# Optimization experiments

Hardware: AMD Instinct MI355X
Metric: run time of the kernel (lower is better)

The kernel has to match this reference:

```python
import jax, jax.numpy as jnp
import numpy as np

N_NODES = 100000
N_EDGES = 1600000
D_FEAT = 64
EPS = 1e-07


def setup_inputs() -> dict:
    key = jax.random.key(0)
    k1, k2, k3 = jax.random.split(key, 3)
    x = jax.random.normal(k1, (N_NODES, D_FEAT), dtype=jnp.float32)
    beta = jnp.ones((1,), dtype=jnp.float32)
    edge_row = jnp.sort(jax.random.randint(k2, (N_EDGES,), 0, N_NODES, dtype=jnp.int64))
    edge_col = jax.random.randint(k3, (N_EDGES,), 0, N_NODES, dtype=jnp.int64)
    return {"x": x, "beta": beta, "edge_row": edge_row, "edge_col": edge_col}


def reference(x, beta, edge_row, edge_col):
    # Gather endpoint features: [E, d]
    A = x[edge_row]
    B = x[edge_col]
    # Cosine similarity per edge, scaled by beta: [E]
    inner = jnp.sum(A * B, axis=1)
    norms = jnp.linalg.norm(A, axis=1) * jnp.linalg.norm(B, axis=1)
    sim = beta[0] * (inner / (norms + EPS))
    # Sparse row-wise softmax (tf.sparse.softmax): stable segment softmax over edges grouped by row
    row_max = jax.ops.segment_max(sim, edge_row, num_segments=N_NODES)
    e = jnp.exp(sim - row_max[edge_row])
    row_sum = jax.ops.segment_sum(e, edge_row, num_segments=N_NODES)
    p = e / row_sum[edge_row]  # [E]
    # SPMM: out[i] = sum_{(i,j) in E} p_ij * x[j]
    out = jax.ops.segment_sum(p[:, None] * B, edge_row, num_segments=N_NODES)
    return out
```

## Files before the change

### kernel.cpp

```cpp
#include <hip/hip_runtime.h>
#include <math.h>

#define D_FEAT 64
typedef _Float16 v8h __attribute__((ext_vector_type(8)));
typedef float v4f __attribute__((ext_vector_type(4)));
typedef _Float16 h2 __attribute__((ext_vector_type(2)));

__device__ __forceinline__ v8h u2h8(uint4 u) { v8h v; __builtin_memcpy(&v, &u, 16); return v; }

__global__ __launch_bounds__(256)
void agnn_prep(const float* __restrict__ x, float* __restrict__ rn,
               uint2* __restrict__ xh, const int* __restrict__ edge_row,
               int* __restrict__ row_ptr, int n_nodes, int n_edges, int nb_prep) {
    if ((int)blockIdx.x < nb_prep) {
        int t = blockIdx.x * blockDim.x + threadIdx.x;
        int node = t >> 4;
        if (node >= n_nodes) return;
        int l4 = t & 15;
        float4 v = ((const float4*)x)[node * 16 + l4];
        float ss = v.x*v.x + v.y*v.y + v.z*v.z + v.w*v.w;
        #pragma unroll
        for (int off = 1; off < 16; off <<= 1) ss += __shfl_xor(ss, off, 64);
        if (l4 == 0) rn[node] = ss > 0.f ? rsqrtf(ss) : 0.f;
        h2 h0 = {(_Float16)v.x, (_Float16)v.y};
        h2 h1 = {(_Float16)v.z, (_Float16)v.w};
        uint2 u;
        __builtin_memcpy(&u.x, &h0, 4);
        __builtin_memcpy(&u.y, &h1, 4);
        xh[node * 16 + l4] = u;
    } else {
        int e = (blockIdx.x - nb_prep) * blockDim.x + threadIdx.x;
        if (e >= n_edges) return;
        int r1 = edge_row[e];
        int r0 = (e == 0) ? -1 : edge_row[e - 1];
        for (int r = r0 + 1; r <= r1; ++r) row_ptr[r] = e;
        if (e == n_edges - 1)
            for (int r = r1 + 1; r <= n_nodes; ++r) row_ptr[r] = n_edges;
    }
}

#define XCP_PITCH 144
#define P_PITCH    80
#define WAVE_LDS  (32 * XCP_PITCH + 16 * P_PITCH)

__global__ __launch_bounds__(64)
void agnn_fused(const float* __restrict__ beta_p,
                const int* __restrict__ edge_col,
                const int* __restrict__ row_ptr,
                const float* __restrict__ rn,
                const uint4* __restrict__ xh4,
                float* __restrict__ out, int n_nodes) {
    __shared__ char lds_raw[WAVE_LDS];
    int lane = threadIdx.x & 63;
    int q    = lane >> 4;
    int lo4  = lane & 15;
    char* XCP = lds_raw;
    char* PL  = XCP + 32 * XCP_PITCH;

    int tile = blockIdx.x;
    int t0 = tile * 16;
    if (t0 >= n_nodes) return;

    int qnode = t0 + lo4; if (qnode >= n_nodes) qnode = n_nodes - 1;
    v8h a0 = u2h8(xh4[(size_t)qnode * 8 + q]);
    v8h a1 = u2h8(xh4[(size_t)qnode * 8 + 4 + q]);

    float beta  = beta_p[0];
    float shift = fabsf(beta);
    int rb = t0 + q * 4;
    float brn0, brn1, brn2, brn3;
    if (t0 + 16 <= n_nodes) {
        float4 rq = *(const float4*)(rn + rb);
        brn0 = beta * rq.x; brn1 = beta * rq.y; brn2 = beta * rq.z; brn3 = beta * rq.w;
    } else {
        brn0 = beta * rn[min(rb + 0, n_nodes - 1)];
        brn1 = beta * rn[min(rb + 1, n_nodes - 1)];
        brn2 = beta * rn[min(rb + 2, n_nodes - 1)];
        brn3 = beta * rn[min(rb + 3, n_nodes - 1)];
    }

    int es   = row_ptr[t0];
    int tend = t0 + 16; if (tend > n_nodes) tend = n_nodes;
    int L    = row_ptr[tend] - es;

    int b0 = row_ptr[min(rb + 0, n_nodes)] - es;
    int b1 = row_ptr[min(rb + 1, n_nodes)] - es;
    int b2 = row_ptr[min(rb + 2, n_nodes)] - es;
    int b3 = row_ptr[min(rb + 3, n_nodes)] - es;
    int b4 = row_ptr[min(rb + 4, n_nodes)] - es;

    v4f o0 = {0,0,0,0}, o1 = {0,0,0,0}, o2 = {0,0,0,0}, o3 = {0,0,0,0};
    float l0 = 0.f, l1 = 0.f, l2 = 0.f, l3 = 0.f;
    unsigned int selp = (lo4 & 1) ? 0x07060302u : 0x05040100u;

    int nch = (L + 31) >> 5;
    if (nch > 0) {
        int cc0, cc1;
        {
            int i0 = lo4, i1 = lo4 + 16;
            cc0 = edge_col[es + (i0 < L ? i0 : 0)];
            cc1 = edge_col[es + (i1 < L ? i1 : 0)];
        }
        float rc0 = rn[cc0], rc1 = rn[cc1];
        uint4 A00 = xh4[(size_t)cc0 * 8 + q];
        uint4 A01 = xh4[(size_t)cc0 * 8 + 4 + q];
        uint4 A10 = xh4[(size_t)cc1 * 8 + q];
        uint4 A11 = xh4[(size_t)cc1 * 8 + 4 + q];

        for (int ch = 0; ch < nch; ++ch) {
            int base = ch << 5;
            bool more = (ch + 1) < nch;

            int nc0, nc1;
            if (more) {
                int i0 = base + 32 + lo4, i1 = i0 + 16;
                nc0 = edge_col[es + (i0 < L ? i0 : 0)];
                nc1 = edge_col[es + (i1 < L ? i1 : 0)];
            } else { nc0 = cc0; nc1 = cc1; }

            v4f z0 = {0,0,0,0};
            z0 = __builtin_amdgcn_mfma_f32_16x16x32_f16(a0, u2h8(A00), z0, 0, 0, 0);
            z0 = __builtin_amdgcn_mfma_f32_16x16x32_f16(a1, u2h8(A01), z0, 0, 0, 0);
            v4f z1 = {0,0,0,0};
            z1 = __builtin_amdgcn_mfma_f32_16x16x32_f16(a0, u2h8(A10), z1, 0, 0, 0);
            z1 = __builtin_amdgcn_mfma_f32_16x16x32_f16(a1, u2h8(A11), z1, 0, 0, 0);

            {
                unsigned int colA = lo4 * 4, colB = (16 + lo4) * 4;
                char* pA = XCP + (4 * q) * XCP_PITCH;
                char* pB = XCP + (16 + 4 * q) * XCP_PITCH;
                *(unsigned int*)(pA + 0 * XCP_PITCH + colA) = A00.x;
                *(unsigned int*)(pA + 1 * XCP_PITCH + colA) = A00.y;
                *(unsigned int*)(pA + 2 * XCP_PITCH + colA) = A00.z;
                *(unsigned int*)(pA + 3 * XCP_PITCH + colA) = A00.w;
                *(unsigned int*)(pB + 0 * XCP_PITCH + colA) = A01.x;
                *(unsigned int*)(pB + 1 * XCP_PITCH + colA) = A01.y;
                *(unsigned int*)(pB + 2 * XCP_PITCH + colA) = A01.z;
                *(unsigned int*)(pB + 3 * XCP_PITCH + colA) = A01.w;
                *(unsigned int*)(pA + 0 * XCP_PITCH + colB) = A10.x;
                *(unsigned int*)(pA + 1 * XCP_PITCH + colB) = A10.y;
                *(unsigned int*)(pA + 2 * XCP_PITCH + colB) = A10.z;
                *(unsigned int*)(pA + 3 * XCP_PITCH + colB) = A10.w;
                *(unsigned int*)(pB + 0 * XCP_PITCH + colB) = A11.x;
                *(unsigned int*)(pB + 1 * XCP_PITCH + colB) = A11.y;
                *(unsigned int*)(pB + 2 * XCP_PITCH + colB) = A11.z;
                *(unsigned int*)(pB + 3 * XCP_PITCH + colB) = A11.w;
            }

            float nr0, nr1; uint4 B00, B01, B10, B11;
            if (more) {
                nr0 = rn[nc0]; nr1 = rn[nc1];
                B00 = xh4[(size_t)nc0 * 8 + q];
                B01 = xh4[(size_t)nc0 * 8 + 4 + q];
                B10 = xh4[(size_t)nc1 * 8 + q];
                B11 = xh4[(size_t)nc1 * 8 + 4 + q];
            } else {
                nr0 = rc0; nr1 = rc1;
                B00 = A00; B01 = A01; B10 = A10; B11 = A11;
            }

            int i0g = base + lo4, i1g = i0g + 16;
            float w00 = (i0g >= b0 && i0g < b1) ? __expf(brn0 * rc0 * z0[0] - shift) : 0.f;
            float w01 = (i0g >= b1 && i0g < b2) ? __expf(brn1 * rc0 * z0[1] - shift) : 0.f;
            float w02 = (i0g >= b2 && i0g < b3) ? __expf(brn2 * rc0 * z0[2] - shift) : 0.f;
            float w03 = (i0g >= b3 && i0g < b4) ? __expf(brn3 * rc0 * z0[3] - shift) : 0.f;
            float w10 = (i1g >= b0 && i1g < b1) ? __expf(brn0 * rc1 * z1[0] - shift) : 0.f;
            float w11 = (i1g >= b1 && i1g < b2) ? __expf(brn1 * rc1 * z1[1] - shift) : 0.f;
            float w12 = (i1g >= b2 && i1g < b3) ? __expf(brn2 * rc1 * z1[2] - shift) : 0.f;
            float w13 = (i1g >= b3 && i1g < b4) ? __expf(brn3 * rc1 * z1[3] - shift) : 0.f;
            l0 += w00 + w10; l1 += w01 + w11; l2 += w02 + w12; l3 += w03 + w13;

            {
                unsigned int cA = lo4 * 2, cB = (16 + lo4) * 2;
                char* pm = PL + (q * 4) * P_PITCH;
                *(_Float16*)(pm + 0 * P_PITCH + cA) = (_Float16)w00;
                *(_Float16*)(pm + 1 * P_PITCH + cA) = (_Float16)w01;
                *(_Float16*)(pm + 2 * P_PITCH + cA) = (_Float16)w02;
                *(_Float16*)(pm + 3 * P_PITCH + cA) = (_Float16)w03;
                *(_Float16*)(pm + 0 * P_PITCH + cB) = (_Float16)w10;
                *(_Float16*)(pm + 1 * P_PITCH + cB) = (_Float16)w11;
                *(_Float16*)(pm + 2 * P_PITCH + cB) = (_Float16)w12;
                *(_Float16*)(pm + 3 * P_PITCH + cB) = (_Float16)w13;
            }

            v8h pah = u2h8(*(const uint4*)(PL + lo4 * P_PITCH + q * 16));
            {
                const char* rp = XCP + (0 + (lo4 >> 1)) * XCP_PITCH + q * 32;
                uint4 da = *(const uint4*)rp;
                uint4 db = *(const uint4*)(rp + 16);
                uint4 bb = { __builtin_amdgcn_perm(da.y, da.x, selp),
                             __builtin_amdgcn_perm(da.w, da.z, selp),
                             __builtin_amdgcn_perm(db.y, db.x, selp),
                             __builtin_amdgcn_perm(db.w, db.z, selp) };
                o0 = __builtin_amdgcn_mfma_f32_16x16x32_f16(pah, u2h8(bb), o0, 0, 0, 0);
            }
            {
                const char* rp = XCP + (8 + (lo4 >> 1)) * XCP_PITCH + q * 32;
                uint4 da = *(const uint4*)rp;
                uint4 db = *(const uint4*)(rp + 16);
                uint4 bb = { __builtin_amdgcn_perm(da.y, da.x, selp),
                             __builtin_amdgcn_perm(da.w, da.z, selp),
                             __builtin_amdgcn_perm(db.y, db.x, selp),
                             __builtin_amdgcn_perm(db.w, db.z, selp) };
                o1 = __builtin_amdgcn_mfma_f32_16x16x32_f16(pah, u2h8(bb), o1, 0, 0, 0);
            }
            {
                const char* rp = XCP + (16 + (lo4 >> 1)) * XCP_PITCH + q * 32;
                uint4 da = *(const uint4*)rp;
                uint4 db = *(const uint4*)(rp + 16);
                uint4 bb = { __builtin_amdgcn_perm(da.y, da.x, selp),
                             __builtin_amdgcn_perm(da.w, da.z, selp),
                             __builtin_amdgcn_perm(db.y, db.x, selp),
                             __builtin_amdgcn_perm(db.w, db.z, selp) };
                o2 = __builtin_amdgcn_mfma_f32_16x16x32_f16(pah, u2h8(bb), o2, 0, 0, 0);
            }
            {
                const char* rp = XCP + (24 + (lo4 >> 1)) * XCP_PITCH + q * 32;
                uint4 da = *(const uint4*)rp;
                uint4 db = *(const uint4*)(rp + 16);
                uint4 bb = { __builtin_amdgcn_perm(da.y, da.x, selp),
                             __builtin_amdgcn_perm(da.w, da.z, selp),
                             __builtin_amdgcn_perm(db.y, db.x, selp),
                             __builtin_amdgcn_perm(db.w, db.z, selp) };
                o3 = __builtin_amdgcn_mfma_f32_16x16x32_f16(pah, u2h8(bb), o3, 0, 0, 0);
            }

            cc0 = nc0; cc1 = nc1; rc0 = nr0; rc1 = nr1;
            A00 = B00; A01 = B01; A10 = B10; A11 = B11;
        }
    }

    #pragma unroll
    for (int off = 1; off < 16; off <<= 1) {
        l0 += __shfl_xor(l0, off, 64);
        l1 += __shfl_xor(l1, off, 64);
        l2 += __shfl_xor(l2, off, 64);
        l3 += __shfl_xor(l3, off, 64);
    }
    float i0 = l0 > 0.f ? 1.f / l0 : 0.f;
    float i1 = l1 > 0.f ? 1.f / l1 : 0.f;
    float i2 = l2 > 0.f ? 1.f / l2 : 0.f;
    float i3 = l3 > 0.f ? 1.f / l3 : 0.f;

    int m0 = rb;
    if (m0 + 0 < n_nodes) { float* p = out + (size_t)(m0 + 0) * 64 + lo4;
        p[0] = o0[0]*i0; p[16] = o1[0]*i0; p[32] = o2[0]*i0; p[48] = o3[0]*i0; }
    if (m0 + 1 < n_nodes) { float* p = out + (size_t)(m0 + 1) * 64 + lo4;
        p[0] = o0[1]*i1; p[16] = o1[1]*i1; p[32] = o2[1]*i1; p[48] = o3[1]*i1; }
    if (m0 + 2 < n_nodes) { float* p = out + (size_t)(m0 + 2) * 64 + lo4;
        p[0] = o0[2]*i2; p[16] = o1[2]*i2; p[32] = o2[2]*i2; p[48] = o3[2]*i2; }
    if (m0 + 3 < n_nodes) { float* p = out + (size_t)(m0 + 3) * 64 + lo4;
        p[0] = o0[3]*i3; p[16] = o1[3]*i3; p[32] = o2[3]*i3; p[48] = o3[3]*i3; }
}

extern "C" void kernel_launch(void* const* d_in, const int* in_sizes, int n_in,
                              void* d_out, int out_size, void* d_ws, size_t ws_size,
                              hipStream_t stream) {
    const float* x        = (const float*)d_in[0];
    const float* beta     = (const float*)d_in[1];
    const int*   edge_row = (const int*)d_in[2];
    const int*   edge_col = (const int*)d_in[3];
    float* out = (float*)d_out;

    int n_nodes = in_sizes[0] / D_FEAT;
    int n_edges = in_sizes[2];

    char* ws = (char*)d_ws;
    float* rn = (float*)ws;
    size_t off0 = ((size_t)n_nodes * sizeof(float) + 255) & ~(size_t)255;
    int* row_ptr = (int*)(ws + off0);
    size_t off1 = off0 + (((size_t)(n_nodes + 1) * sizeof(int) + 255) & ~(size_t)255);
    uint2* xh = (uint2*)(ws + off1);

    {
        int nb_prep = (n_nodes * 16 + 255) / 256;
        int nb_rp   = (n_edges + 255) / 256;
        agnn_prep<<<nb_prep + nb_rp, 256, 0, stream>>>(
            x, rn, xh, edge_row, row_ptr, n_nodes, n_edges, nb_prep);
    }
    {
        int tiles = (n_nodes + 15) / 16;
        agnn_fused<<<tiles, 64, 0, stream>>>(beta, edge_col, row_ptr,
                                             rn, (const uint4*)xh, out, n_nodes);
    }
}
```

Measured before the change: 127.3 us.

## Split each tile's edge chunks across two waves and merge partials in LDS

The fused kernel now runs two waves per 16-node tile. Each wave takes alternating 32-edge chunks and keeps its own LDS staging area. The second wave then writes its partial accumulators and softmax denominators to LDS, and the first wave adds them in before normalising and storing. This doubles the parallelism per tile to hide gather latency on the roughly 256 edges per tile, at the cost of a block-wide barrier, extra LDS traffic and duplicated per-tile setup loads.

```diff
diff --git a/kernel.cpp b/kernel.cpp
--- a/kernel.cpp
+++ b/kernel.cpp
@@ -43,23 +43,23 @@
 #define P_PITCH    80
 #define WAVE_LDS  (32 * XCP_PITCH + 16 * P_PITCH)
 
-__global__ __launch_bounds__(64)
+__global__ __launch_bounds__(128)
 void agnn_fused(const float* __restrict__ beta_p,
                 const int* __restrict__ edge_col,
                 const int* __restrict__ row_ptr,
                 const float* __restrict__ rn,
                 const uint4* __restrict__ xh4,
                 float* __restrict__ out, int n_nodes) {
-    __shared__ char lds_raw[WAVE_LDS];
+    __shared__ char lds_raw[2 * WAVE_LDS];
+    int wid  = threadIdx.x >> 6;
     int lane = threadIdx.x & 63;
     int q    = lane >> 4;
     int lo4  = lane & 15;
-    char* XCP = lds_raw;
+    char* XCP = lds_raw + wid * WAVE_LDS;
     char* PL  = XCP + 32 * XCP_PITCH;
 
     int tile = blockIdx.x;
     int t0 = tile * 16;
-    if (t0 >= n_nodes) return;
 
     int qnode = t0 + lo4; if (qnode >= n_nodes) qnode = n_nodes - 1;
     v8h a0 = u2h8(xh4[(size_t)qnode * 8 + q]);
@@ -93,11 +93,12 @@
     float l0 = 0.f, l1 = 0.f, l2 = 0.f, l3 = 0.f;
     unsigned int selp = (lo4 & 1) ? 0x07060302u : 0x05040100u;
 
-    int nch = (L + 31) >> 5;
-    if (nch > 0) {
+    int nch  = (L + 31) >> 5;
+    int nchw = (nch > wid) ? ((nch - wid + 1) >> 1) : 0;
+    if (nchw > 0) {
         int cc0, cc1;
         {
-            int i0 = lo4, i1 = lo4 + 16;
+            int i0 = (wid << 5) + lo4, i1 = i0 + 16;
             cc0 = edge_col[es + (i0 < L ? i0 : 0)];
             cc1 = edge_col[es + (i1 < L ? i1 : 0)];
         }
@@ -107,13 +108,13 @@
         uint4 A10 = xh4[(size_t)cc1 * 8 + q];
         uint4 A11 = xh4[(size_t)cc1 * 8 + 4 + q];
 
-        for (int ch = 0; ch < nch; ++ch) {
-            int base = ch << 5;
-            bool more = (ch + 1) < nch;
+        for (int k = 0; k < nchw; ++k) {
+            int base = (wid + 2 * k) << 5;
+            bool more = (k + 1) < nchw;
 
             int nc0, nc1;
             if (more) {
-                int i0 = base + 32 + lo4, i1 = i0 + 16;
+                int i0 = base + 64 + lo4, i1 = i0 + 16;
                 nc0 = edge_col[es + (i0 < L ? i0 : 0)];
                 nc1 = edge_col[es + (i1 < L ? i1 : 0)];
             } else { nc0 = cc0; nc1 = cc1; }
@@ -230,6 +231,27 @@
         }
     }
 
+    if (wid == 1) {
+        char* ST = XCP;
+        *(v4f*)(ST + lane * 80 +  0) = o0;
+        *(v4f*)(ST + lane * 80 + 16) = o1;
+        *(v4f*)(ST + lane * 80 + 32) = o2;
+        *(v4f*)(ST + lane * 80 + 48) = o3;
+        float4 lv = {l0, l1, l2, l3};
+        *(float4*)(ST + lane * 80 + 64) = lv;
+    }
+    __syncthreads();
+    if (wid == 1) return;
+    {
+        const char* ST = lds_raw + WAVE_LDS;
+        o0 += *(const v4f*)(ST + lane * 80 +  0);
+        o1 += *(const v4f*)(ST + lane * 80 + 16);
+        o2 += *(const v4f*)(ST + lane * 80 + 32);
+        o3 += *(const v4f*)(ST + lane * 80 + 48);
+        float4 lv = *(const float4*)(ST + lane * 80 + 64);
+        l0 += lv.x; l1 += lv.y; l2 += lv.z; l3 += lv.w;
+    }
+
     #pragma unroll
     for (int off = 1; off < 16; off <<= 1) {
         l0 += __shfl_xor(l0, off, 64);
@@ -280,7 +302,7 @@
     }
     {
         int tiles = (n_nodes + 15) / 16;
-        agnn_fused<<<tiles, 64, 0, stream>>>(beta, edge_col, row_ptr,
-                                             rn, (const uint4*)xh, out, n_nodes);
+        agnn_fused<<<tiles, 128, 0, stream>>>(beta, edge_col, row_ptr,
+                                              rn, (const uint4*)xh, out, n_nodes);
     }
 }
```

Result: no change. 125.4 us (-1.4%).
